# Performance work log

Measured on AMD Instinct MI355X. Metric: run time of the kernel, lower is better.

## Reference

```python
import jax, jax.numpy as jnp
import numpy as np

N_TOPICS = 1024
TOPIC_DIM = 128
HIDDEN = 512
N_HEADS = 8
HEAD_DIM = HIDDEN // N_HEADS
N_LAYERS = 2
ALPHA = 0.2
TIME_DECAY = 0.1
BATCH = 8


def setup_inputs() -> dict:
    key = jax.random.key(0)
    ks = jax.random.split(key, 16)
    inp = {
        'topic_ids': jax.random.randint(ks[0], (BATCH,), 0, N_TOPICS, dtype=jnp.int32),
        'adj_matrix': jax.random.randint(ks[1], (BATCH, N_TOPICS, N_TOPICS), 0, 2, dtype=jnp.int32),
        'time_matrix': jax.random.uniform(ks[2], (BATCH, N_TOPICS, N_TOPICS), dtype=jnp.float32),
        'attractiveness': jax.random.normal(ks[3], (BATCH,), dtype=jnp.float32),
        # parameters (torch Linear convention: W [out,in], y = x@W.T + b)
        'topic_embedding': jax.random.normal(ks[4], (N_TOPICS, TOPIC_DIM), dtype=jnp.float32) * 0.1,
        'struct_W': jax.random.normal(ks[5], (HIDDEN, TOPIC_DIM), dtype=jnp.float32) * 0.05,
        'struct_b': jnp.zeros((HIDDEN,), dtype=jnp.float32),
        'attract_W': jax.random.normal(ks[6], (HIDDEN, 1), dtype=jnp.float32) * 0.05,
        'attract_b': jnp.zeros((HIDDEN,), dtype=jnp.float32),
        'gat_W': jax.random.normal(ks[7], (N_LAYERS, N_HEADS, HIDDEN, HEAD_DIM), dtype=jnp.float32) * 0.05,
        'gat_a': jax.random.normal(ks[8], (N_LAYERS, N_HEADS, 2 * HEAD_DIM, 1), dtype=jnp.float32) * 0.05,
        'fc1_W': jax.random.normal(ks[9], (HIDDEN, HIDDEN), dtype=jnp.float32) * 0.05,
        'fc1_b': jnp.zeros((HIDDEN,), dtype=jnp.float32),
        'fc2_W': jax.random.normal(ks[10], (1, HIDDEN), dtype=jnp.float32) * 0.05,
        'fc2_b': jnp.zeros((1,), dtype=jnp.float32),
    }
    return inp


def _gat_layer(node, adj, time_w, W, a):
    # node: [B,N,F], adj: [B,N,N] (0/1), time_w: [B,N,N]
    # W: [H,F,hd], a: [H,2*hd,1]
    h = jnp.einsum('bni,hio->bhno', node, W)  # [B,H,N,hd]
    # Additive attention: a = [a_src; a_dst] so e_ij = LeakyReLU(h_i.a_src + h_j.a_dst)
    a_src = a[:, :HEAD_DIM, 0]   # [H,hd]
    a_dst = a[:, HEAD_DIM:, 0]   # [H,hd]
    e_src = jnp.einsum('bhnd,hd->bhn', h, a_src)  # [B,H,N]
    e_dst = jnp.einsum('bhnd,hd->bhn', h, a_dst)  # [B,H,N]
    e = e_src[:, :, :, None] + e_dst[:, :, None, :]  # [B,H,N,N]
    e = jax.nn.leaky_relu(e, negative_slope=ALPHA)
    e = e * time_w[:, None, :, :]
    e = jnp.where(adj[:, None, :, :] == 0, -jnp.inf, e)
    attn = jax.nn.softmax(e, axis=-1)
    out = jnp.einsum('bhij,bhjd->bhid', attn, h)  # [B,H,N,hd]
    out = out.transpose(0, 2, 1, 3).reshape(node.shape[0], node.shape[1], -1)
    return jax.nn.elu(out)


def reference(topic_ids, adj_matrix, time_matrix, attractiveness,
              topic_embedding, struct_W, struct_b, attract_W, attract_b,
              gat_W, gat_a, fc1_W, fc1_b, fc2_W, fc2_b):
    # structural features for all topics -> hidden
    struct = topic_embedding @ struct_W.T + struct_b          # [N,hidden]
    attract = attractiveness[:, None] @ attract_W.T + attract_b  # [B,hidden]
    node = jnp.broadcast_to(struct[None], (BATCH, N_TOPICS, HIDDEN))
    # weighted co-occurrence time (eq.17)
    time_w = jnp.exp(-TIME_DECAY * (time_matrix.max() - time_matrix))  # [B,N,N]
    for l in range(N_LAYERS):
        node = _gat_layer(node, adj_matrix, time_w, gat_W[l], gat_a[l])
    # gather per-sample topic node feature
    topic_feat = jnp.take_along_axis(node, topic_ids[:, None, None].astype(jnp.int32), axis=1)[:, 0]  # [B,hidden]
    combined = topic_feat + attract
    hidden = jax.nn.relu(combined @ fc1_W.T + fc1_b)
    pred = hidden @ fc2_W.T + fc2_b  # [B,1]
    return pred
```

## Files before the change

kernel.cpp:

```cpp
#include <hip/hip_runtime.h>

#define NT 1024
#define TD 128
#define HID 512
#define NH 8
#define HD 64
#define NB 8

typedef unsigned short us;
typedef short bf16x8 __attribute__((ext_vector_type(8)));
typedef float f32x4 __attribute__((ext_vector_type(4)));

#define LOG2E 1.44269504f

__device__ __forceinline__ us f2bf(float x) {
    unsigned int u = __float_as_uint(x);
    return (us)((u + 0x7FFFu + ((u >> 16) & 1u)) >> 16);
}
__device__ __forceinline__ float bf2f(us s) {
    return __uint_as_float(((unsigned int)s) << 16);
}

__global__ __launch_bounds__(256) void kprep(const float* __restrict__ tm, float* __restrict__ part,
                                             const float* __restrict__ emb, const float* __restrict__ sW,
                                             const float* __restrict__ sb, us* __restrict__ node0b,
                                             const float* __restrict__ gW, us* __restrict__ Wt,
                                             const float* __restrict__ fc2b, float* __restrict__ out) {
    __shared__ __align__(16) float smf[8768];
    int bx = blockIdx.x, t = threadIdx.x;
    if (bx < 1024) {
        const float4* tm4 = (const float4*)tm;
        size_t base = (size_t)bx * 256 + t;
        float m = -1e30f;
        #pragma unroll
        for (int k = 0; k < 8; k++) {
            float4 v = tm4[base + (size_t)k * 262144];
            m = fmaxf(m, fmaxf(fmaxf(v.x, v.y), fmaxf(v.z, v.w)));
        }
        smf[t] = m; __syncthreads();
        for (int s = 128; s > 0; s >>= 1) { if (t < s) smf[t] = fmaxf(smf[t], smf[t + s]); __syncthreads(); }
        if (t == 0) part[bx] = smf[0];
    } else if (bx < 1152) {
        int g = bx - 1024; int iblk = g & 15, oseg = g >> 4;
        us* As = (us*)smf;
        us* Bs = (us*)smf + 64 * 136;
        const float4* esrc = (const float4*)(emb + (size_t)iblk * 64 * TD);
        const float4* wsrc = (const float4*)(sW + (size_t)oseg * 64 * TD);
        #pragma unroll
        for (int rep = 0; rep < 8; rep++) {
            int f = rep * 256 + t;
            int row = f >> 5, c4 = f & 31;
            float4 av = esrc[f];
            float4 bv = wsrc[f];
            us pa[4] = {f2bf(av.x), f2bf(av.y), f2bf(av.z), f2bf(av.w)};
            us pb[4] = {f2bf(bv.x), f2bf(bv.y), f2bf(bv.z), f2bf(bv.w)};
            *(uint2*)&As[row * 136 + c4 * 4] = *(uint2*)pa;
            *(uint2*)&Bs[row * 136 + c4 * 4] = *(uint2*)pb;
        }
        __syncthreads();
        int l = t & 63, w = t >> 6, m = l & 15, q = l >> 4;
        f32x4 acc[4];
        #pragma unroll
        for (int ot = 0; ot < 4; ot++) acc[ot] = (f32x4){0.f, 0.f, 0.f, 0.f};
        #pragma unroll
        for (int ks = 0; ks < 4; ks++) {
            bf16x8 a = *(const bf16x8*)&As[(w * 16 + m) * 136 + ks * 32 + q * 8];
            #pragma unroll
            for (int ot = 0; ot < 4; ot++) {
                bf16x8 b = *(const bf16x8*)&Bs[(ot * 16 + m) * 136 + ks * 32 + q * 8];
                acc[ot] = __builtin_amdgcn_mfma_f32_16x16x32_bf16(a, b, acc[ot], 0, 0, 0);
            }
        }
        #pragma unroll
        for (int ot = 0; ot < 4; ot++) {
            int col = oseg * 64 + ot * 16 + m;
            float sbv = sb[col];
            #pragma unroll
            for (int rr = 0; rr < 4; rr++) {
                int rowi = iblk * 64 + w * 16 + q * 4 + rr;
                node0b[(size_t)rowi * HID + col] = f2bf(acc[ot][rr] + sbv);
            }
        }
    } else {
        int g = bx - 1152; int lh = g >> 3, kt = g & 7;
        if (g == 0 && t < NB) out[t] = fc2b[0];
        float* tile = smf;
        const float4* src = (const float4*)(gW + ((size_t)lh * HID + kt * 64) * HD);
        #pragma unroll
        for (int rep = 0; rep < 4; rep++) {
            int f = rep * 256 + t;
            float4 v = src[f];
            int row = f >> 4, col = (f & 15) * 4;
            float* d = tile + row * 65 + col;
            d[0] = v.x; d[1] = v.y; d[2] = v.z; d[3] = v.w;
        }
        __syncthreads();
        int o = t >> 2, ks = (t & 3) * 16;
        us pk[16];
        #pragma unroll
        for (int j = 0; j < 16; j++) pk[j] = f2bf(tile[(ks + j) * 65 + o]);
        us* dst = Wt + (size_t)lh * HD * HID + (size_t)o * HID + kt * 64 + ks;
        *(uint4*)dst = *(uint4*)pk;
        *(uint4*)(dst + 8) = *(uint4*)&pk[8];
    }
}

__device__ __forceinline__ void gemm_body(const us* __restrict__ A, const us* __restrict__ W,
                                          const float* __restrict__ gav,
                                          us* __restrict__ outT, us* __restrict__ outR,
                                          float* __restrict__ esO, float* __restrict__ edO,
                                          int iblk, int b, int h, int t, us* sm) {
    us* As = sm;
    us* Bs = sm + 2 * 4608;
    int row = t >> 2, ks = t & 3;
    int l = t & 63, w = t >> 6, m = l & 15, q = l >> 4;
    size_t arow0 = (size_t)(b * NT + iblk * 64);
    const us* ar = A + (arow0 + row) * HID + ks * 16;
    const us* br = W + ((size_t)(h * HD + row)) * HID + ks * 16;
    f32x4 acc[4];
    #pragma unroll
    for (int ot = 0; ot < 4; ot++) acc[ot] = (f32x4){0.f, 0.f, 0.f, 0.f};
    {
        uint4 x0 = *(const uint4*)ar, x1 = *(const uint4*)(ar + 8);
        uint4 y0 = *(const uint4*)br, y1 = *(const uint4*)(br + 8);
        *(uint4*)&As[row * 72 + ks * 16] = x0; *(uint4*)&As[row * 72 + ks * 16 + 8] = x1;
        *(uint4*)&Bs[row * 72 + ks * 16] = y0; *(uint4*)&Bs[row * 72 + ks * 16 + 8] = y1;
    }
    uint4 a0 = *(const uint4*)(ar + 64), a1 = *(const uint4*)(ar + 72);
    uint4 b0 = *(const uint4*)(br + 64), b1 = *(const uint4*)(br + 72);
    for (int it = 0; it < 8; it++) {
        int cur = it & 1, nxt = cur ^ 1;
        uint4 na0, na1, nb0, nb1;
        if (it < 6) {
            int k0 = (it + 2) * 64;
            na0 = *(const uint4*)(ar + k0); na1 = *(const uint4*)(ar + k0 + 8);
            nb0 = *(const uint4*)(br + k0); nb1 = *(const uint4*)(br + k0 + 8);
        }
        __syncthreads();
        if (it < 7) {
            *(uint4*)&As[nxt * 4608 + row * 72 + ks * 16] = a0;
            *(uint4*)&As[nxt * 4608 + row * 72 + ks * 16 + 8] = a1;
            *(uint4*)&Bs[nxt * 4608 + row * 72 + ks * 16] = b0;
            *(uint4*)&Bs[nxt * 4608 + row * 72 + ks * 16 + 8] = b1;
        }
        const us* Ac = As + cur * 4608; const us* Bc = Bs + cur * 4608;
        #pragma unroll
        for (int kt = 0; kt < 2; kt++) {
            bf16x8 av = *(const bf16x8*)&Ac[(w * 16 + m) * 72 + kt * 32 + q * 8];
            #pragma unroll
            for (int ot = 0; ot < 4; ot++) {
                bf16x8 bv = *(const bf16x8*)&Bc[(ot * 16 + m) * 72 + kt * 32 + q * 8];
                acc[ot] = __builtin_amdgcn_mfma_f32_16x16x32_bf16(av, bv, acc[ot], 0, 0, 0);
            }
        }
        if (it < 6) { a0 = na0; a1 = na1; b0 = nb0; b1 = nb1; }
    }
    const float* gas = gav + h * 2 * HD;
    float gs[4], gd[4];
    #pragma unroll
    for (int ot = 0; ot < 4; ot++) { gs[ot] = gas[ot * 16 + m]; gd[ot] = gas[HD + ot * 16 + m]; }
    size_t ebase = ((size_t)b * NH + h) * NT + iblk * 64;
    #pragma unroll
    for (int rr = 0; rr < 4; rr++) {
        float s = 0.f, d = 0.f;
        #pragma unroll
        for (int ot = 0; ot < 4; ot++) { float v = acc[ot][rr]; s = fmaf(v, gs[ot], s); d = fmaf(v, gd[ot], d); }
        #pragma unroll
        for (int mask = 1; mask < 16; mask <<= 1) { s += __shfl_xor(s, mask); d += __shfl_xor(d, mask); }
        if (m == 0) {
            int rowi = w * 16 + q * 4 + rr;
            esO[ebase + rowi] = s;
            edO[ebase + rowi] = d;
        }
    }
    #pragma unroll
    for (int ot = 0; ot < 4; ot++) {
        int col = h * HD + ot * 16 + m;
        #pragma unroll
        for (int rr = 0; rr < 4; rr++) {
            int i_loc = w * 16 + q * 4 + rr;
            float v = acc[ot][rr];
            if (outT) outT[(size_t)col * NT + iblk * 64 + i_loc] = f2bf(v);
            if (outR) outR[(arow0 + i_loc) * HID + col] = f2bf(v);
        }
    }
}

__global__ __launch_bounds__(256) void kphase1(const float* __restrict__ tm, const int* __restrict__ adj,
                                               const float* __restrict__ part, us* __restrict__ TWb,
                                               const us* __restrict__ node0b, const us* __restrict__ Wt,
                                               const float* __restrict__ ga, us* __restrict__ Ht1,
                                               float* __restrict__ es1, float* __restrict__ ed1) {
    __shared__ __align__(16) us sm[4 * 4608];
    int bx = blockIdx.x, t = threadIdx.x;
    if (bx < 2048) {
        float* red = (float*)sm;
        float m = fmaxf(fmaxf(part[t * 4], part[t * 4 + 1]), fmaxf(part[t * 4 + 2], part[t * 4 + 3]));
        red[t] = m; __syncthreads();
        for (int s = 128; s > 0; s >>= 1) { if (t < s) red[t] = fmaxf(red[t], red[t + s]); __syncthreads(); }
        float tmx = red[0];
        const float C = 0.1f * LOG2E;
        #pragma unroll
        for (int it = 0; it < 4; it++) {
            size_t idx = (((size_t)bx * 4 + it) * 256 + t) * 4;
            float4 tv = *(const float4*)(tm + idx);
            int4 av = *(const int4*)(adj + idx);
            float w0 = exp2f((tv.x - tmx) * C) * LOG2E;
            float w1 = exp2f((tv.y - tmx) * C) * LOG2E;
            float w2 = exp2f((tv.z - tmx) * C) * LOG2E;
            float w3 = exp2f((tv.w - tmx) * C) * LOG2E;
            unsigned int fa = av.x ? __float_as_uint(w0) : 0x7FC00000u;
            unsigned int fb = av.y ? __float_as_uint(w1) : 0x7FC00000u;
            unsigned int fc = av.z ? __float_as_uint(w2) : 0x7FC00000u;
            unsigned int fd = av.w ? __float_as_uint(w3) : 0x7FC00000u;
            uint2 pk;
            pk.x = __builtin_amdgcn_perm(fb, fa, 0x07060302);
            pk.y = __builtin_amdgcn_perm(fd, fc, 0x07060302);
            *(uint2*)&TWb[idx] = pk;
        }
    } else {
        int g = bx - 2048;
        gemm_body(node0b, Wt, ga, Ht1, nullptr, es1, ed1, g & 15, 0, g >> 4, t, sm);
    }
}

__global__ __launch_bounds__(256) void kedge(const float* __restrict__ es, const float* __restrict__ ed,
                                             us* __restrict__ E1) {
    int g = blockIdx.x;
    int h = g >> 8, i0 = (g & 255) << 2;
    int t = threadIdx.x;
    __shared__ float eds[NT];
    *(float4*)&eds[t * 4] = *(const float4*)&ed[h * NT + t * 4];
    __syncthreads();
    int j = t * 4;
    float4 e4 = *(const float4*)&eds[j];
    #pragma unroll
    for (int r = 0; r < 4; r++) {
        float esv = es[h * NT + i0 + r];
        float a = esv + e4.x; a = fmaxf(a, 0.2f * a);
        float bq = esv + e4.y; bq = fmaxf(bq, 0.2f * bq);
        float c = esv + e4.z; c = fmaxf(c, 0.2f * c);
        float d = esv + e4.w; d = fmaxf(d, 0.2f * d);
        uint2 pk;
        pk.x = __builtin_amdgcn_perm(__float_as_uint(bq), __float_as_uint(a), 0x07060302);
        pk.y = __builtin_amdgcn_perm(__float_as_uint(d), __float_as_uint(c), 0x07060302);
        *(uint2*)&E1[((size_t)(h * NT) + i0 + r) * NT + j] = pk;
    }
}

__global__ __launch_bounds__(256) void kgemm2(const us* __restrict__ node1b, const us* __restrict__ Wt2,
                                              const float* __restrict__ ga2, us* __restrict__ H2b,
                                              float* __restrict__ es2, float* __restrict__ ed2) {
    __shared__ __align__(16) us sm[4 * 4608];
    int x = blockIdx.x;
    gemm_body(node1b, Wt2, ga2, nullptr, H2b, es2, ed2, x & 15, x >> 4, blockIdx.y, threadIdx.x, sm);
}

__device__ __forceinline__ void compute_p(uint4 T0, uint4 T1, uint4 E0, uint4 E1v,
                                          uint4& P01, uint4& P23) {
    union U { uint4 v; unsigned int w[4]; };
    U t0; t0.v = T0; U t1; t1.v = T1; U e0; e0.v = E0; U e1; e1.v = E1v;
    unsigned int pk[8];
    #pragma unroll
    for (int r = 0; r < 4; r++) {
        float twa = __uint_as_float(t0.w[r] << 16);
        float twb = __uint_as_float(t0.w[r] & 0xFFFF0000u);
        float Ea  = __uint_as_float(e0.w[r] << 16);
        float Eb  = __uint_as_float(e0.w[r] & 0xFFFF0000u);
        float pa = fmaxf(exp2f(twa * Ea), 0.f);
        float pb = fmaxf(exp2f(twb * Eb), 0.f);
        pk[r] = __builtin_amdgcn_perm(__float_as_uint(pb), __float_as_uint(pa), 0x07060302);
    }
    #pragma unroll
    for (int r = 0; r < 4; r++) {
        float twa = __uint_as_float(t1.w[r] << 16);
        float twb = __uint_as_float(t1.w[r] & 0xFFFF0000u);
        float Ea  = __uint_as_float(e1.w[r] << 16);
        float Eb  = __uint_as_float(e1.w[r] & 0xFFFF0000u);
        float pa = fmaxf(exp2f(twa * Ea), 0.f);
        float pb = fmaxf(exp2f(twb * Eb), 0.f);
        pk[4 + r] = __builtin_amdgcn_perm(__float_as_uint(pb), __float_as_uint(pa), 0x07060302);
    }
    P01 = make_uint4(pk[0], pk[1], pk[2], pk[3]);
    P23 = make_uint4(pk[4], pk[5], pk[6], pk[7]);
}

__global__ __launch_bounds__(256) void kattn1(const us* __restrict__ TWb, const us* __restrict__ Ht,
                                              const us* __restrict__ E1, us* __restrict__ node1b) {
    int x = blockIdx.x; int iblk = x & 15; int b = x >> 4; int h = blockIdx.y;
    int t = threadIdx.x;
    __shared__ __align__(16) us Ps[2 * 4608];
    __shared__ __align__(16) us Hs[2 * 4608];
    __shared__ float invl_s[64];
    int i = t >> 2, js = t & 3;
    int l = t & 63, w = t >> 6, m = l & 15, q = l >> 4;
    const us* twrow = TWb + ((size_t)(b * NT) + iblk * 64 + i) * NT + js * 16;
    const us* erow  = E1 + ((size_t)(h * NT) + iblk * 64 + i) * NT + js * 16;
    const us* htrow = Ht + ((size_t)(h * HD) + i) * NT + js * 16;
    f32x4 acc[4];
    #pragma unroll
    for (int ot = 0; ot < 4; ot++) acc[ot] = (f32x4){0.f, 0.f, 0.f, 0.f};
    f32x4 acc1 = (f32x4){0.f, 0.f, 0.f, 0.f};
    short ov = (m == 0) ? (short)0x3F80 : (short)0;
    bf16x8 bones = {ov, ov, ov, ov, ov, ov, ov, ov};
    uint4 T0, T1, E0, E1r, Hh0, Hh1;
    T0 = *(const uint4*)twrow; T1 = *(const uint4*)(twrow + 8);
    E0 = *(const uint4*)erow;  E1r = *(const uint4*)(erow + 8);
    Hh0 = *(const uint4*)htrow; Hh1 = *(const uint4*)(htrow + 8);
    {
        uint4 p01, p23;
        compute_p(T0, T1, E0, E1r, p01, p23);
        us* Pd = Ps + i * 72 + js * 16;
        us* Hd = Hs + i * 72 + js * 16;
        *(uint4*)Pd = p01; *(uint4*)(Pd + 8) = p23;
        *(uint4*)Hd = Hh0; *(uint4*)(Hd + 8) = Hh1;
    }
    T0 = *(const uint4*)(twrow + 64); T1 = *(const uint4*)(twrow + 72);
    E0 = *(const uint4*)(erow + 64);  E1r = *(const uint4*)(erow + 72);
    Hh0 = *(const uint4*)(htrow + 64); Hh1 = *(const uint4*)(htrow + 72);
    for (int it = 0; it < 16; it++) {
        int cur = it & 1, nxt = cur ^ 1;
        uint4 nT0, nT1, nE0, nE1, nH0, nH1;
        if (it < 14) {
            int j0 = (it + 2) * 64;
            nT0 = *(const uint4*)(twrow + j0); nT1 = *(const uint4*)(twrow + j0 + 8);
            nE0 = *(const uint4*)(erow + j0);  nE1 = *(const uint4*)(erow + j0 + 8);
            nH0 = *(const uint4*)(htrow + j0); nH1 = *(const uint4*)(htrow + j0 + 8);
        }
        uint4 p01, p23;
        if (it < 15) compute_p(T0, T1, E0, E1r, p01, p23);
        __syncthreads();
        if (it < 15) {
            us* Pd = Ps + nxt * 4608 + i * 72 + js * 16;
            us* Hd = Hs + nxt * 4608 + i * 72 + js * 16;
            *(uint4*)Pd = p01; *(uint4*)(Pd + 8) = p23;
            *(uint4*)Hd = Hh0; *(uint4*)(Hd + 8) = Hh1;
        }
        const us* Pc = Ps + cur * 4608; const us* Hc = Hs + cur * 4608;
        #pragma unroll
        for (int kt = 0; kt < 2; kt++) {
            bf16x8 av = *(const bf16x8*)&Pc[(w * 16 + m) * 72 + kt * 32 + q * 8];
            #pragma unroll
            for (int ot = 0; ot < 4; ot++) {
                bf16x8 bv = *(const bf16x8*)&Hc[(ot * 16 + m) * 72 + kt * 32 + q * 8];
                acc[ot] = __builtin_amdgcn_mfma_f32_16x16x32_bf16(av, bv, acc[ot], 0, 0, 0);
            }
            acc1 = __builtin_amdgcn_mfma_f32_16x16x32_bf16(av, bones, acc1, 0, 0, 0);
        }
        if (it < 14) { T0 = nT0; T1 = nT1; E0 = nE0; E1r = nE1; Hh0 = nH0; Hh1 = nH1; }
    }
    if (m == 0) {
        #pragma unroll
        for (int rr = 0; rr < 4; rr++) invl_s[w * 16 + q * 4 + rr] = 1.f / acc1[rr];
    }
    __syncthreads();
    #pragma unroll
    for (int ot = 0; ot < 4; ot++) {
        int col = h * HD + ot * 16 + m;
        #pragma unroll
        for (int rr = 0; rr < 4; rr++) {
            int i_loc = w * 16 + q * 4 + rr;
            float v = acc[ot][rr] * invl_s[i_loc];
            v = v > 0.f ? v : (__expf(v) - 1.f);
            node1b[(size_t)(b * NT + iblk * 64 + i_loc) * HID + col] = f2bf(v);
        }
    }
}

__global__ __launch_bounds__(256) void kattn2a(const us* __restrict__ TWb, const us* __restrict__ H2b,
                                               const float* __restrict__ es2, const float* __restrict__ ed2,
                                               const int* __restrict__ topic_ids,
                                               float* __restrict__ ppv, float* __restrict__ pl) {
    int js = blockIdx.x, h = blockIdx.y, b = blockIdx.z;
    int t = threadIdx.x;
    __shared__ float pls[64];
    __shared__ float red[256];
    int qi = topic_ids[b];
    if (t < 64) {
        int j = js * 64 + t;
        float esq = es2[((size_t)b * NH + h) * NT + qi];
        float tw = bf2f(TWb[((size_t)(b * NT) + qi) * NT + j]);
        float e = esq + ed2[((size_t)b * NH + h) * NT + j];
        e = fmaxf(e, 0.2f * e) * tw;
        float p = fmaxf(exp2f(e), 0.f);
        pls[t] = p;
        float lsum = p;
        #pragma unroll
        for (int mask = 1; mask < 64; mask <<= 1) lsum += __shfl_xor(lsum, mask);
        if (t == 0) pl[((size_t)b * NH + h) * 16 + js] = lsum;
    }
    __syncthreads();
    int o = t & 63, jg = t >> 6;
    float acc = 0.f;
    const us* hb = H2b + ((size_t)(b * NT) + js * 64 + jg * 16) * HID + h * HD + o;
    #pragma unroll
    for (int jj = 0; jj < 16; jj++)
        acc = fmaf(pls[jg * 16 + jj], bf2f(hb[(size_t)jj * HID]), acc);
    red[t] = acc; __syncthreads();
    if (t < 64) {
        float pv = red[t] + red[t + 64] + red[t + 128] + red[t + 192];
        ppv[(((size_t)b * NH + h) * 16 + js) * HD + t] = pv;
    }
}

__global__ __launch_bounds__(256) void khead2(const float* __restrict__ ppv, const float* __restrict__ pl,
                                              const float* __restrict__ attr,
                                              const float* __restrict__ aW, const float* __restrict__ ab,
                                              const float* __restrict__ fc1W, const float* __restrict__ fc1b,
                                              const float* __restrict__ fc2W, float* __restrict__ out) {
    int kseg = blockIdx.x, b = blockIdx.y;
    int t = threadIdx.x;
    __shared__ float comb[HID];
    __shared__ float linv[NH];
    __shared__ float r2[256];
    if (t < NH) {
        float lsum = 0.f;
        #pragma unroll
        for (int js = 0; js < 16; js++) lsum += pl[((size_t)b * NH + t) * 16 + js];
        linv[t] = 1.f / lsum;
    }
    __syncthreads();
    float av = attr[b];
    for (int k = t; k < HID; k += 256) {
        int h = k >> 6, o = k & 63;
        float pv = 0.f;
        #pragma unroll
        for (int js = 0; js < 16; js++) pv += ppv[(((size_t)b * NH + h) * 16 + js) * HD + o];
        float v = pv * linv[h];
        v = v > 0.f ? v : (__expf(v) - 1.f);
        comb[k] = v + av * aW[k] + ab[k];
    }
    __syncthreads();
    int kk = kseg * 16 + (t >> 4);
    int j = t & 15;
    const float* row = fc1W + (size_t)kk * HID;
    float acc = 0.f;
    #pragma unroll 8
    for (int mi = 0; mi < 32; mi++) {
        int idx = mi * 16 + j;
        acc = fmaf(comb[idx], row[idx], acc);
    }
    #pragma unroll
    for (int mask = 1; mask < 16; mask <<= 1) acc += __shfl_xor(acc, mask);
    float partv = 0.f;
    if (j == 0) {
        float hk = fmaxf(acc + fc1b[kk], 0.f);
        partv = hk * fc2W[kk];
    }
    r2[t] = partv; __syncthreads();
    for (int s = 128; s > 0; s >>= 1) { if (t < s) r2[t] += r2[t + s]; __syncthreads(); }
    if (t == 0) atomicAdd(&out[b], r2[0]);
}

extern "C" void kernel_launch(void* const* d_in, const int* in_sizes, int n_in,
                              void* d_out, int out_size, void* d_ws, size_t ws_size,
                              hipStream_t stream) {
    const int*   topic_ids = (const int*)d_in[0];
    const int*   adj       = (const int*)d_in[1];
    const float* tm        = (const float*)d_in[2];
    const float* attr      = (const float*)d_in[3];
    const float* emb       = (const float*)d_in[4];
    const float* sW        = (const float*)d_in[5];
    const float* sb        = (const float*)d_in[6];
    const float* aW        = (const float*)d_in[7];
    const float* ab        = (const float*)d_in[8];
    const float* gW        = (const float*)d_in[9];
    const float* ga        = (const float*)d_in[10];
    const float* fc1W      = (const float*)d_in[11];
    const float* fc1b      = (const float*)d_in[12];
    const float* fc2W      = (const float*)d_in[13];
    const float* fc2b      = (const float*)d_in[14];
    float* out = (float*)d_out;

    char* p = (char*)d_ws;
    us* TWb    = (us*)p; p += sizeof(us) * (size_t)NB * NT * NT;
    us* E1     = (us*)p; p += sizeof(us) * (size_t)NH * NT * NT;
    us* node0b = (us*)p; p += sizeof(us) * (size_t)NT * HID;
    us* Wt     = (us*)p; p += sizeof(us) * (size_t)2 * NH * HD * HID;
    us* Ht1    = (us*)p; p += sizeof(us) * (size_t)HID * NT;
    us* node1b = (us*)p; p += sizeof(us) * (size_t)NB * NT * HID;
    us* H2b    = (us*)p; p += sizeof(us) * (size_t)NB * NT * HID;
    float* es1  = (float*)p; p += sizeof(float) * NH * NT;
    float* ed1  = (float*)p; p += sizeof(float) * NH * NT;
    float* es2  = (float*)p; p += sizeof(float) * NB * NH * NT;
    float* ed2  = (float*)p; p += sizeof(float) * NB * NH * NT;
    float* ppv  = (float*)p; p += sizeof(float) * NB * NH * 16 * HD;
    float* pl   = (float*)p; p += sizeof(float) * NB * NH * 16;
    float* part = (float*)p; p += sizeof(float) * 1024;

    kprep<<<1280, 256, 0, stream>>>(tm, part, emb, sW, sb, node0b, gW, Wt, fc2b, out);
    kphase1<<<2176, 256, 0, stream>>>(tm, adj, part, TWb, node0b, Wt, ga, Ht1, es1, ed1);
    kedge<<<2048, 256, 0, stream>>>(es1, ed1, E1);
    kattn1<<<dim3(16 * NB, NH), 256, 0, stream>>>(TWb, Ht1, E1, node1b);
    kgemm2<<<dim3(16 * NB, NH), 256, 0, stream>>>(node1b, Wt + (size_t)NH * HD * HID,
                                                  ga + NH * 2 * HD, H2b, es2, ed2);
    kattn2a<<<dim3(16, NH, NB), 256, 0, stream>>>(TWb, H2b, es2, ed2, topic_ids, ppv, pl);
    khead2<<<dim3(32, NB), 256, 0, stream>>>(ppv, pl, attr, aW, ab, fc1W, fc1b, fc2W, out);
}
```

Measured before the change: 203.1 us.

## Fold layer-2 attention scores into attn1 and fuse gemm2 with query attention

Precomputes W2·a_src/a_dst vectors per head so layer-2 e_src/e_dst can be accumulated with atomics directly in the layer-1 attention epilogue. This removes the need to compute them after gemm2. kgemm2 then fuses the query-row softmax-weighted reduction, which eliminates the H2b buffer write/read and the kattn2a launch. Zeroing of the atomic accumulators is folded into kphase1. The change adds many atomics and changes float summation order.

```diff
diff --git a/kernel.cpp b/kernel.cpp
--- a/kernel.cpp
+++ b/kernel.cpp
@@ -25,6 +25,7 @@
                                              const float* __restrict__ emb, const float* __restrict__ sW,
                                              const float* __restrict__ sb, us* __restrict__ node0b,
                                              const float* __restrict__ gW, us* __restrict__ Wt,
+                                             const float* __restrict__ ga, float* __restrict__ ws2,
                                              const float* __restrict__ fc2b, float* __restrict__ out) {
     __shared__ __align__(16) float smf[8768];
     int bx = blockIdx.x, t = threadIdx.x;
@@ -81,9 +82,8 @@
                 node0b[(size_t)rowi * HID + col] = f2bf(acc[ot][rr] + sbv);
             }
         }
-    } else {
+    } else if (bx < 1280) {
         int g = bx - 1152; int lh = g >> 3, kt = g & 7;
-        if (g == 0 && t < NB) out[t] = fc2b[0];
         float* tile = smf;
         const float4* src = (const float4*)(gW + ((size_t)lh * HID + kt * 64) * HD);
         #pragma unroll
@@ -102,12 +102,31 @@
         us* dst = Wt + (size_t)lh * HD * HID + (size_t)o * HID + kt * 64 + ks;
         *(uint4*)dst = *(uint4*)pk;
         *(uint4*)(dst + 8) = *(uint4*)&pk[8];
+    } else {
+        int hp = bx - 1280;
+        if (hp == 0 && t < NB) out[t] = fc2b[0];
+        const float* gsrc = ga + (size_t)(NH + hp) * 2 * HD;
+        const float* wbase = gW + (size_t)(NH + hp) * HID * HD;
+        #pragma unroll
+        for (int rep = 0; rep < 2; rep++) {
+            int k = rep * 256 + t;
+            const float* wr = wbase + (size_t)k * HD;
+            float s = 0.f, d = 0.f;
+            #pragma unroll 8
+            for (int o = 0; o < HD; o++) {
+                float wv = wr[o];
+                s = fmaf(wv, gsrc[o], s);
+                d = fmaf(wv, gsrc[HD + o], d);
+            }
+            ws2[hp * HID + k] = s;
+            ws2[(8 + hp) * HID + k] = d;
+        }
     }
 }
 
 __device__ __forceinline__ void gemm_body(const us* __restrict__ A, const us* __restrict__ W,
                                           const float* __restrict__ gav,
-                                          us* __restrict__ outT, us* __restrict__ outR,
+                                          us* __restrict__ outT,
                                           float* __restrict__ esO, float* __restrict__ edO,
                                           int iblk, int b, int h, int t, us* sm) {
     us* As = sm;
@@ -179,18 +198,18 @@
         #pragma unroll
         for (int rr = 0; rr < 4; rr++) {
             int i_loc = w * 16 + q * 4 + rr;
-            float v = acc[ot][rr];
-            if (outT) outT[(size_t)col * NT + iblk * 64 + i_loc] = f2bf(v);
-            if (outR) outR[(arow0 + i_loc) * HID + col] = f2bf(v);
-        }
-    }
-}
-
+            outT[(size_t)col * NT + iblk * 64 + i_loc] = f2bf(acc[ot][rr]);
+        }
+    }
+}
+
+#define ZF4 33808
 __global__ __launch_bounds__(256) void kphase1(const float* __restrict__ tm, const int* __restrict__ adj,
                                                const float* __restrict__ part, us* __restrict__ TWb,
                                                const us* __restrict__ node0b, const us* __restrict__ Wt,
                                                const float* __restrict__ ga, us* __restrict__ Ht1,
-                                               float* __restrict__ es1, float* __restrict__ ed1) {
+                                               float* __restrict__ es1, float* __restrict__ ed1,
+                                               float* __restrict__ zbase) {
     __shared__ __align__(16) us sm[4 * 4608];
     int bx = blockIdx.x, t = threadIdx.x;
     if (bx < 2048) {
@@ -218,9 +237,12 @@
             pk.y = __builtin_amdgcn_perm(fd, fc, 0x07060302);
             *(uint2*)&TWb[idx] = pk;
         }
+    } else if (bx < 2176) {
+        int g = bx - 2048;
+        gemm_body(node0b, Wt, ga, Ht1, es1, ed1, g & 15, 0, g >> 4, t, sm);
     } else {
-        int g = bx - 2048;
-        gemm_body(node0b, Wt, ga, Ht1, nullptr, es1, ed1, g & 15, 0, g >> 4, t, sm);
+        size_t idx = (size_t)(bx - 2176) * 256 + t;
+        if (idx < ZF4) ((float4*)zbase)[idx] = (float4){0.f, 0.f, 0.f, 0.f};
     }
 }
 
@@ -248,14 +270,6 @@
     }
 }
 
-__global__ __launch_bounds__(256) void kgemm2(const us* __restrict__ node1b, const us* __restrict__ Wt2,
-                                              const float* __restrict__ ga2, us* __restrict__ H2b,
-                                              float* __restrict__ es2, float* __restrict__ ed2) {
-    __shared__ __align__(16) us sm[4 * 4608];
-    int x = blockIdx.x;
-    gemm_body(node1b, Wt2, ga2, nullptr, H2b, es2, ed2, x & 15, x >> 4, blockIdx.y, threadIdx.x, sm);
-}
-
 __device__ __forceinline__ void compute_p(uint4 T0, uint4 T1, uint4 E0, uint4 E1v,
                                           uint4& P01, uint4& P23) {
     union U { uint4 v; unsigned int w[4]; };
@@ -286,7 +300,9 @@
 }
 
 __global__ __launch_bounds__(256) void kattn1(const us* __restrict__ TWb, const us* __restrict__ Ht,
-                                              const us* __restrict__ E1, us* __restrict__ node1b) {
+                                              const us* __restrict__ E1, const float* __restrict__ ws2,
+                                              us* __restrict__ node1b,
+                                              float* __restrict__ es2, float* __restrict__ ed2) {
     int x = blockIdx.x; int iblk = x & 15; int b = x >> 4; int h = blockIdx.y;
     int t = threadIdx.x;
     __shared__ __align__(16) us Ps[2 * 4608];
@@ -354,6 +370,7 @@
         for (int rr = 0; rr < 4; rr++) invl_s[w * 16 + q * 4 + rr] = 1.f / acc1[rr];
     }
     __syncthreads();
+    float varr[4][4];
     #pragma unroll
     for (int ot = 0; ot < 4; ot++) {
         int col = h * HD + ot * 16 + m;
@@ -362,48 +379,126 @@
             int i_loc = w * 16 + q * 4 + rr;
             float v = acc[ot][rr] * invl_s[i_loc];
             v = v > 0.f ? v : (__expf(v) - 1.f);
+            varr[ot][rr] = v;
             node1b[(size_t)(b * NT + iblk * 64 + i_loc) * HID + col] = f2bf(v);
         }
     }
-}
-
-__global__ __launch_bounds__(256) void kattn2a(const us* __restrict__ TWb, const us* __restrict__ H2b,
-                                               const float* __restrict__ es2, const float* __restrict__ ed2,
-                                               const int* __restrict__ topic_ids,
-                                               float* __restrict__ ppv, float* __restrict__ pl) {
-    int js = blockIdx.x, h = blockIdx.y, b = blockIdx.z;
+    #pragma unroll
+    for (int h2 = 0; h2 < NH; h2++) {
+        float wsv[4], wdv[4];
+        #pragma unroll
+        for (int ot = 0; ot < 4; ot++) {
+            int col = h * HD + ot * 16 + m;
+            wsv[ot] = ws2[h2 * HID + col];
+            wdv[ot] = ws2[(8 + h2) * HID + col];
+        }
+        #pragma unroll
+        for (int rr = 0; rr < 4; rr++) {
+            float s = 0.f, d = 0.f;
+            #pragma unroll
+            for (int ot = 0; ot < 4; ot++) { s = fmaf(varr[ot][rr], wsv[ot], s); d = fmaf(varr[ot][rr], wdv[ot], d); }
+            #pragma unroll
+            for (int mask = 1; mask < 16; mask <<= 1) { s += __shfl_xor(s, mask); d += __shfl_xor(d, mask); }
+            if (m == 0) {
+                int ig = iblk * 64 + w * 16 + q * 4 + rr;
+                atomicAdd(&es2[(size_t)(b * NH + h2) * NT + ig], s);
+                atomicAdd(&ed2[(size_t)(b * NH + h2) * NT + ig], d);
+            }
+        }
+    }
+}
+
+__global__ __launch_bounds__(256) void kgemm2(const us* __restrict__ node1b, const us* __restrict__ Wt2,
+                                              const us* __restrict__ TWb,
+                                              const float* __restrict__ es2, const float* __restrict__ ed2,
+                                              const int* __restrict__ topic_ids,
+                                              float* __restrict__ pv, float* __restrict__ pl) {
+    __shared__ __align__(16) us sm[4 * 4608];
+    __shared__ float pv_s[4][64];
+    __shared__ float pl_s[4];
+    int x = blockIdx.x; int iblk = x & 15; int b = x >> 4; int h = blockIdx.y;
     int t = threadIdx.x;
-    __shared__ float pls[64];
-    __shared__ float red[256];
+    us* As = sm;
+    us* Bs = sm + 2 * 4608;
+    int row = t >> 2, ks = t & 3;
+    int l = t & 63, w = t >> 6, m = l & 15, q = l >> 4;
+    size_t arow0 = (size_t)(b * NT + iblk * 64);
+    const us* ar = node1b + (arow0 + row) * HID + ks * 16;
+    const us* br = Wt2 + ((size_t)(h * HD + row)) * HID + ks * 16;
+    f32x4 acc[4];
+    #pragma unroll
+    for (int ot = 0; ot < 4; ot++) acc[ot] = (f32x4){0.f, 0.f, 0.f, 0.f};
+    {
+        uint4 x0 = *(const uint4*)ar, x1 = *(const uint4*)(ar + 8);
+        uint4 y0 = *(const uint4*)br, y1 = *(const uint4*)(br + 8);
+        *(uint4*)&As[row * 72 + ks * 16] = x0; *(uint4*)&As[row * 72 + ks * 16 + 8] = x1;
+        *(uint4*)&Bs[row * 72 + ks * 16] = y0; *(uint4*)&Bs[row * 72 + ks * 16 + 8] = y1;
+    }
+    uint4 a0 = *(const uint4*)(ar + 64), a1 = *(const uint4*)(ar + 72);
+    uint4 b0 = *(const uint4*)(br + 64), b1 = *(const uint4*)(br + 72);
+    for (int it = 0; it < 8; it++) {
+        int cur = it & 1, nxt = cur ^ 1;
+        uint4 na0, na1, nb0, nb1;
+        if (it < 6) {
+            int k0 = (it + 2) * 64;
+            na0 = *(const uint4*)(ar + k0); na1 = *(const uint4*)(ar + k0 + 8);
+            nb0 = *(const uint4*)(br + k0); nb1 = *(const uint4*)(br + k0 + 8);
+        }
+        __syncthreads();
+        if (it < 7) {
+            *(uint4*)&As[nxt * 4608 + row * 72 + ks * 16] = a0;
+            *(uint4*)&As[nxt * 4608 + row * 72 + ks * 16 + 8] = a1;
+            *(uint4*)&Bs[nxt * 4608 + row * 72 + ks * 16] = b0;
+            *(uint4*)&Bs[nxt * 4608 + row * 72 + ks * 16 + 8] = b1;
+        }
+        const us* Ac = As + cur * 4608; const us* Bc = Bs + cur * 4608;
+        #pragma unroll
+        for (int kt = 0; kt < 2; kt++) {
+            bf16x8 av = *(const bf16x8*)&Ac[(w * 16 + m) * 72 + kt * 32 + q * 8];
+            #pragma unroll
+            for (int ot = 0; ot < 4; ot++) {
+                bf16x8 bv = *(const bf16x8*)&Bc[(ot * 16 + m) * 72 + kt * 32 + q * 8];
+                acc[ot] = __builtin_amdgcn_mfma_f32_16x16x32_bf16(av, bv, acc[ot], 0, 0, 0);
+            }
+        }
+        if (it < 6) { a0 = na0; a1 = na1; b0 = nb0; b1 = nb1; }
+    }
     int qi = topic_ids[b];
+    float es_q = es2[(size_t)(b * NH + h) * NT + qi];
+    float pvp[4] = {0.f, 0.f, 0.f, 0.f};
+    float psum = 0.f;
+    #pragma unroll
+    for (int rr = 0; rr < 4; rr++) {
+        int j = iblk * 64 + w * 16 + q * 4 + rr;
+        float edj = ed2[(size_t)(b * NH + h) * NT + j];
+        float tw = bf2f(TWb[((size_t)(b * NT) + qi) * NT + j]);
+        float e = es_q + edj;
+        e = fmaxf(e, 0.2f * e) * tw;
+        float pj = fmaxf(exp2f(e), 0.f);
+        psum += pj;
+        #pragma unroll
+        for (int ot = 0; ot < 4; ot++) pvp[ot] = fmaf(pj, acc[ot][rr], pvp[ot]);
+    }
+    #pragma unroll
+    for (int mask = 16; mask < 64; mask <<= 1) {
+        psum += __shfl_xor(psum, mask);
+        #pragma unroll
+        for (int ot = 0; ot < 4; ot++) pvp[ot] += __shfl_xor(pvp[ot], mask);
+    }
+    if (q == 0) {
+        #pragma unroll
+        for (int ot = 0; ot < 4; ot++) pv_s[w][ot * 16 + m] = pvp[ot];
+        if (m == 0) pl_s[w] = psum;
+    }
+    __syncthreads();
     if (t < 64) {
-        int j = js * 64 + t;
-        float esq = es2[((size_t)b * NH + h) * NT + qi];
-        float tw = bf2f(TWb[((size_t)(b * NT) + qi) * NT + j]);
-        float e = esq + ed2[((size_t)b * NH + h) * NT + j];
-        e = fmaxf(e, 0.2f * e) * tw;
-        float p = fmaxf(exp2f(e), 0.f);
-        pls[t] = p;
-        float lsum = p;
-        #pragma unroll
-        for (int mask = 1; mask < 64; mask <<= 1) lsum += __shfl_xor(lsum, mask);
-        if (t == 0) pl[((size_t)b * NH + h) * 16 + js] = lsum;
-    }
-    __syncthreads();
-    int o = t & 63, jg = t >> 6;
-    float acc = 0.f;
-    const us* hb = H2b + ((size_t)(b * NT) + js * 64 + jg * 16) * HID + h * HD + o;
-    #pragma unroll
-    for (int jj = 0; jj < 16; jj++)
-        acc = fmaf(pls[jg * 16 + jj], bf2f(hb[(size_t)jj * HID]), acc);
-    red[t] = acc; __syncthreads();
-    if (t < 64) {
-        float pv = red[t] + red[t + 64] + red[t + 128] + red[t + 192];
-        ppv[(((size_t)b * NH + h) * 16 + js) * HD + t] = pv;
-    }
-}
-
-__global__ __launch_bounds__(256) void khead2(const float* __restrict__ ppv, const float* __restrict__ pl,
+        float s = pv_s[0][t] + pv_s[1][t] + pv_s[2][t] + pv_s[3][t];
+        atomicAdd(&pv[(size_t)(b * NH + h) * HD + t], s);
+    }
+    if (t == 0) atomicAdd(&pl[b * NH + h], pl_s[0] + pl_s[1] + pl_s[2] + pl_s[3]);
+}
+
+__global__ __launch_bounds__(256) void khead2(const float* __restrict__ pv, const float* __restrict__ pl,
                                               const float* __restrict__ attr,
                                               const float* __restrict__ aW, const float* __restrict__ ab,
                                               const float* __restrict__ fc1W, const float* __restrict__ fc1b,
@@ -413,20 +508,12 @@
     __shared__ float comb[HID];
     __shared__ float linv[NH];
     __shared__ float r2[256];
-    if (t < NH) {
-        float lsum = 0.f;
-        #pragma unroll
-        for (int js = 0; js < 16; js++) lsum += pl[((size_t)b * NH + t) * 16 + js];
-        linv[t] = 1.f / lsum;
-    }
+    if (t < NH) linv[t] = 1.f / pl[b * NH + t];
     __syncthreads();
     float av = attr[b];
     for (int k = t; k < HID; k += 256) {
         int h = k >> 6, o = k & 63;
-        float pv = 0.f;
-        #pragma unroll
-        for (int js = 0; js < 16; js++) pv += ppv[(((size_t)b * NH + h) * 16 + js) * HD + o];
-        float v = pv * linv[h];
+        float v = pv[(size_t)(b * NH + h) * HD + o] * linv[h];
         v = v > 0.f ? v : (__expf(v) - 1.f);
         comb[k] = v + av * aW[k] + ab[k];
     }
@@ -479,21 +566,20 @@
     us* Wt     = (us*)p; p += sizeof(us) * (size_t)2 * NH * HD * HID;
     us* Ht1    = (us*)p; p += sizeof(us) * (size_t)HID * NT;
     us* node1b = (us*)p; p += sizeof(us) * (size_t)NB * NT * HID;
-    us* H2b    = (us*)p; p += sizeof(us) * (size_t)NB * NT * HID;
     float* es1  = (float*)p; p += sizeof(float) * NH * NT;
     float* ed1  = (float*)p; p += sizeof(float) * NH * NT;
     float* es2  = (float*)p; p += sizeof(float) * NB * NH * NT;
     float* ed2  = (float*)p; p += sizeof(float) * NB * NH * NT;
-    float* ppv  = (float*)p; p += sizeof(float) * NB * NH * 16 * HD;
-    float* pl   = (float*)p; p += sizeof(float) * NB * NH * 16;
+    float* pv   = (float*)p; p += sizeof(float) * NB * NH * HD;
+    float* pl   = (float*)p; p += sizeof(float) * NB * NH;
+    float* ws2  = (float*)p; p += sizeof(float) * 16 * HID;
     float* part = (float*)p; p += sizeof(float) * 1024;
 
-    kprep<<<1280, 256, 0, stream>>>(tm, part, emb, sW, sb, node0b, gW, Wt, fc2b, out);
-    kphase1<<<2176, 256, 0, stream>>>(tm, adj, part, TWb, node0b, Wt, ga, Ht1, es1, ed1);
+    kprep<<<1288, 256, 0, stream>>>(tm, part, emb, sW, sb, node0b, gW, Wt, ga, ws2, fc2b, out);
+    kphase1<<<2309, 256, 0, stream>>>(tm, adj, part, TWb, node0b, Wt, ga, Ht1, es1, ed1, es2);
     kedge<<<2048, 256, 0, stream>>>(es1, ed1, E1);
-    kattn1<<<dim3(16 * NB, NH), 256, 0, stream>>>(TWb, Ht1, E1, node1b);
-    kgemm2<<<dim3(16 * NB, NH), 256, 0, stream>>>(node1b, Wt + (size_t)NH * HD * HID,
-                                                  ga + NH * 2 * HD, H2b, es2, ed2);
-    kattn2a<<<dim3(16, NH, NB), 256, 0, stream>>>(TWb, H2b, es2, ed2, topic_ids, ppv, pl);
-    khead2<<<dim3(32, NB), 256, 0, stream>>>(ppv, pl, attr, aW, ab, fc1W, fc1b, fc2W, out);
-}
+    kattn1<<<dim3(16 * NB, NH), 256, 0, stream>>>(TWb, Ht1, E1, ws2, node1b, es2, ed2);
+    kgemm2<<<dim3(16 * NB, NH), 256, 0, stream>>>(node1b, Wt + (size_t)NH * HD * HID, TWb,
+                                                  es2, ed2, topic_ids, pv, pl);
+    khead2<<<dim3(32, NB), 256, 0, stream>>>(pv, pl, attr, aW, ab, fc1W, fc1b, fc2W, out);
+}
```

After: 211.9 us. 4.3% more time.
